# Kernel tuning notes

Hardware: AMD Instinct MI355X
Metric: run time of the kernel (lower is better)

## Reference

```python
import jax, jax.numpy as jnp
import numpy as np

N, E, L, HID, HEADS, G = 50000, 800000, 2, 128, 8, 256
DK = HID // HEADS

def _ln(x, g, b, eps=1e-5):
    m = jnp.mean(x, axis=-1, keepdims=True)
    v = jnp.mean((x - m) ** 2, axis=-1, keepdims=True)
    return (x - m) * jax.lax.rsqrt(v + eps) * g + b

def setup_inputs() -> dict:
    key = jax.random.key(0)
    ks = jax.random.split(key, 24)
    rn = lambda i, s: (0.05 * jax.random.normal(ks[i], s)).astype(jnp.float32)
    return {
        'node_attr': jax.random.randint(ks[0], (N, 4), 0, 64, dtype=jnp.int32),
        'batch_idx': jnp.sort(jax.random.randint(ks[1], (N,), 0, G, dtype=jnp.int32)),
        'edge_index': jax.random.randint(ks[2], (2, E), 0, N, dtype=jnp.int32),
        'strat_dist': jax.random.randint(ks[3], (E,), 0, 32, dtype=jnp.int32),
        'strat_path': jax.random.randint(ks[4], (E,), 0, 16, dtype=jnp.int32),
        'atom_emb': rn(5, (4, 64, HID)),
        'dist_emb': rn(6, (L, 32, HID)),
        'path_emb': rn(7, (L, 16, HID)),
        'Wq': rn(8, (L, HID, HID)), 'bq': rn(9, (L, HID)),
        'Wk': rn(10, (L, HID, HID)), 'bk': rn(11, (L, HID)),
        'Wv': rn(12, (L, HID, HID)), 'bv': rn(13, (L, HID)),
        'Wa': rn(14, (L, HID, HID)), 'ba': rn(15, (L, HID)),
        'ln1_g': jnp.ones((L, HID), jnp.float32), 'ln1_b': jnp.zeros((L, HID), jnp.float32),
        'Wmid': rn(16, (L, HID, 2 * HID)), 'bmid': rn(17, (L, 2 * HID)),
        'Wo': rn(18, (L, 2 * HID, HID)), 'bo': rn(19, (L, HID)),
        'ln2_g': jnp.ones((L, HID), jnp.float32), 'ln2_b': jnp.zeros((L, HID), jnp.float32),
        'W_out': rn(20, (HID, 1)), 'b_out': jnp.zeros((1,), jnp.float32),
    }

def reference(node_attr, batch_idx, edge_index, strat_dist, strat_path,
              atom_emb, dist_emb, path_emb, Wq, bq, Wk, bk, Wv, bv, Wa, ba,
              ln1_g, ln1_b, Wmid, bmid, Wo, bo, ln2_g, ln2_b, W_out, b_out):
    # node encoder: sum of per-feature embeddings (AtomEncoder style)
    x = sum(atom_emb[f][node_attr[:, f]] for f in range(node_attr.shape[1]))  # [N, HID]
    src, tgt = edge_index[0], edge_index[1]  # j (source), i (target)
    inv_sqrt_dk = np.float32(1.0 / np.sqrt(DK))
    for l in range(L):
        # per-edge gather + relational encodings added to the source vector
        s = x[src] + dist_emb[l][strat_dist] + path_emb[l][strat_path]  # [E, HID]
        t = x[tgt]                                                      # [E, HID]
        q = (t @ Wq[l] + bq[l]).reshape(E, HEADS, DK)
        k = (s @ Wk[l] + bk[l]).reshape(E, HEADS, DK)
        v = (s @ Wv[l] + bv[l]).reshape(E, HEADS, DK)
        scores = jnp.sum(q * k, axis=-1) * inv_sqrt_dk  # [E, HEADS]
        # segment softmax keyed on target node id
        smax = jax.ops.segment_max(scores, tgt, num_segments=N)
        ex = jnp.exp(scores - smax[tgt])
        den = jax.ops.segment_sum(ex, tgt, num_segments=N)
        att = ex / (den[tgt] + 1e-16)                   # [E, HEADS]
        msg = (v * att[:, :, None]).reshape(E, HID)
        aggr = jax.ops.segment_sum(msg, tgt, num_segments=N)  # scatter-add
        # update: attn FFN + residual + LayerNorms (dropout is identity in eval)
        h = _ln(jax.nn.gelu(aggr, approximate=False) @ Wa[l] + ba[l] + x, ln1_g[l], ln1_b[l])
        h2 = jax.nn.gelu(h @ Wmid[l] + bmid[l], approximate=False) @ Wo[l] + bo[l]
        x = _ln(h2 + h, ln2_g[l], ln2_b[l])
    # global mean pool per graph, then readout
    cnt = jax.ops.segment_sum(jnp.ones((N,), x.dtype), batch_idx, num_segments=G)
    pooled = jax.ops.segment_sum(x, batch_idx, num_segments=G) / jnp.maximum(cnt, 1.0)[:, None]
    return pooled @ W_out + b_out
```

## Files before the change

### kernel.cpp

```cpp
#include <hip/hip_runtime.h>
#include <hip/hip_bf16.h>
#include <math.h>
#include <stdint.h>

#define N_NODES 50000
#define N_EDGES 800000
#define HID 128
#define NGRAPH 256
#define NLAYER 2
#define CAP 64

#define CPAD 5

#define SC_GRP 196
#define SC_B (SC_GRP * 8)
#define NPART 6250

#define ENC_B 3125
#define TKV_B (ENC_B + 1024)
#define RPK_B (TKV_B + 128)
#define PREP_B (RPK_B + 4)

typedef __bf16 bf16x8 __attribute__((ext_vector_type(8)));
typedef __bf16 bf16x2 __attribute__((ext_vector_type(2)));
typedef float f32x4 __attribute__((ext_vector_type(4)));
typedef float f32x2 __attribute__((ext_vector_type(2)));

__device__ __forceinline__ float gelu_f(float v) {
    return 0.5f * v * (1.0f + erff(v * 0.70710678118654752f));
}

__device__ __forceinline__ f32x2 f8lo(uint32_t d) {
    return __builtin_amdgcn_cvt_pk_f32_fp8((int)d, false);
}
__device__ __forceinline__ f32x2 f8hi(uint32_t d) {
    return __builtin_amdgcn_cvt_pk_f32_fp8((int)d, true);
}
__device__ __forceinline__ uint32_t pk4_fp8(float a, float b, float c, float d) {
    int w = __builtin_amdgcn_cvt_pk_fp8_f32(a, b, 0, false);
    w = __builtin_amdgcn_cvt_pk_fp8_f32(c, d, w, true);
    return (uint32_t)w;
}
__device__ __forceinline__ f32x2 bfpair(uint32_t d) {
    f32x2 r;
    r[0] = __uint_as_float(d << 16);
    r[1] = __uint_as_float(d);
    return r;
}

__global__ __launch_bounds__(256) void prep_kernel(
    const int* __restrict__ attr, const float* __restrict__ aemb,
    __bf16* __restrict__ xb,
    const float* __restrict__ de, const float* __restrict__ pe,
    const float* __restrict__ Wk, const float* __restrict__ Wv,
    __bf16* __restrict__ tkv,
    const float* __restrict__ Wq, const float* __restrict__ Wa,
    const float* __restrict__ Wmid, const float* __restrict__ Wo,
    __bf16* __restrict__ wqkvf, __bf16* __restrict__ waf,
    __bf16* __restrict__ wmidf, __bf16* __restrict__ wof,
    const int* __restrict__ batch, const float* __restrict__ bout,
    const float* __restrict__ bq, const float* __restrict__ bk,
    const float* __restrict__ bv,
    float* __restrict__ invc, float* __restrict__ outp, float* __restrict__ bqkv,
    const int* __restrict__ tgt, const int* __restrict__ src,
    const int* __restrict__ sd, const int* __restrict__ sp,
    int* __restrict__ cnt, uint32_t* __restrict__ ei) {
    __shared__ float sde[128];
    int b = blockIdx.x;
    int tid = threadIdx.x;
    if (b < SC_B) {
        int grp = b >> 3;
        int part = b & 7;
        int plo = part * NPART;
        int phi = plo + NPART;
        int base = grp * 4096 + tid;
#pragma unroll
        for (int k = 0; k < 16; k++) {
            int e = base + k * 256;
            if (e < N_EDGES) {
                int t = tgt[e];
                if (t >= plo && t < phi) {
                    uint32_t pk = (uint32_t)src[e] | ((uint32_t)((sd[e] << 4) | sp[e]) << 16);
                    int r = atomicAdd(&cnt[t << CPAD], 1);
                    if (r < CAP) ei[(t << 6) + r] = pk;
                }
            }
        }
        return;
    }
    b -= SC_B;
    if (b < ENC_B) {
        int gid = b * 256 + tid;
        int n = gid >> 4;
        int c8 = (gid & 15) << 3;
        const int4 a = *(const int4*)(attr + n * 4);
        const float* r0 = aemb + (size_t)(0 * 64 + a.x) * 128 + c8;
        const float* r1 = aemb + (size_t)(1 * 64 + a.y) * 128 + c8;
        const float* r2 = aemb + (size_t)(2 * 64 + a.z) * 128 + c8;
        const float* r3 = aemb + (size_t)(3 * 64 + a.w) * 128 + c8;
        f32x4 v0a = *(const f32x4*)r0, v0b = *(const f32x4*)(r0 + 4);
        f32x4 v1a = *(const f32x4*)r1, v1b = *(const f32x4*)(r1 + 4);
        f32x4 v2a = *(const f32x4*)r2, v2b = *(const f32x4*)(r2 + 4);
        f32x4 v3a = *(const f32x4*)r3, v3b = *(const f32x4*)(r3 + 4);
        bf16x8 o;
#pragma unroll
        for (int j = 0; j < 4; j++) {
            o[j] = (__bf16)(v0a[j] + v1a[j] + v2a[j] + v3a[j]);
            o[4 + j] = (__bf16)(v0b[j] + v1b[j] + v2b[j] + v3b[j]);
        }
        *(bf16x8*)(xb + (size_t)n * 128 + c8) = o;
    } else if (b < TKV_B) {
        int bb = b - ENC_B;
        int l = bb >> 9;
        int md = bb & 511;
        int dd = md >> 4, pp = md & 15;
        int c = tid;
        if (c < 128) sde[c] = de[l * 4096 + dd * 128 + c] + pe[l * 2048 + pp * 128 + c];
        __syncthreads();
        const float* W = (c < 128) ? (Wk + l * 16384) : (Wv + l * 16384);
        int cc = c & 127;
        float acc = 0.f;
#pragma unroll 4
        for (int k = 0; k < 128; k++) acc = fmaf(sde[k], W[k * 128 + cc], acc);
        tkv[(size_t)bb * 256 + c] = (__bf16)acc;
    } else if (b < RPK_B) {
        int u = (b - TKV_B) * 256 + tid;
        int l = u >> 14, r = u & 16383;
        const float* srcp;
        __bf16* dstp;
        int kg, scol, srcCO;
        if (r < 6144) {
            kg = r / 384;
            int uu = r % 384;
            int sec = uu >> 7, cc = uu & 127;
            scol = ((cc & 15) << 3) | (cc >> 4);
            const float* Ws = (sec == 0) ? Wq : (sec == 1) ? Wk : Wv;
            srcp = Ws + l * 16384;
            srcCO = 128;
            dstp = wqkvf + (size_t)l * 49152 + (size_t)r * 8;
        } else if (r < 8192) {
            int rr = r - 6144;
            kg = rr >> 7;
            int cc = rr & 127;
            scol = ((cc & 15) << 3) | (cc >> 4);
            srcp = Wa + l * 16384;
            srcCO = 128;
            dstp = waf + (size_t)l * 16384 + (size_t)rr * 8;
        } else if (r < 12288) {
            int rr = r - 8192;
            kg = rr >> 8;
            int uu = rr & 255;
            int blk = uu >> 7, cc = uu & 127;
            scol = blk * 128 + (((cc & 15) << 3) | (cc >> 4));
            srcp = Wmid + l * 32768;
            srcCO = 256;
            dstp = wmidf + (size_t)l * 32768 + (size_t)rr * 8;
        } else {
            int rr = r - 12288;
            kg = rr >> 7;
            int cc = rr & 127;
            scol = ((cc & 15) << 3) | (cc >> 4);
            srcp = Wo + l * 32768;
            srcCO = 128;
            dstp = wof + (size_t)l * 32768 + (size_t)rr * 8;
        }
        bf16x8 o;
#pragma unroll
        for (int j = 0; j < 8; j++) o[j] = (__bf16)srcp[(kg * 8 + j) * srcCO + scol];
        *(bf16x8*)dstp = o;
    } else {
        int sb = b - RPK_B;
        if (sb == 0) {
            int g = tid;
            int lo = 0, hi = N_NODES;
            while (lo < hi) { int mid = (lo + hi) >> 1; if (batch[mid] < g) lo = mid + 1; else hi = mid; }
            int start = lo;
            lo = start; hi = N_NODES;
            while (lo < hi) { int mid = (lo + hi) >> 1; if (batch[mid] < g + 1) lo = mid + 1; else hi = mid; }
            int c2 = lo - start;
            invc[g] = 1.0f / fmaxf((float)c2, 1.0f);
            outp[g] = bout[0];
        } else {
            int r = (sb - 1) * 256 + tid;
            int l = r / 384, c = r % 384;
            float v = (c < 128) ? bq[l * 128 + c]
                    : (c < 256) ? bk[l * 128 + c - 128]
                                : bv[l * 128 + c - 256];
            bqkv[r] = v;
        }
    }
}

__global__ __launch_bounds__(256) void qkv_gemm(
    const __bf16* __restrict__ A, const __bf16* __restrict__ Wf,
    const float* __restrict__ bias, __bf16* __restrict__ Qb,
    uint8_t* __restrict__ kv8, int M) {
    int tid = threadIdx.x;
    int bq = blockIdx.x;
    int sec = bq % 3;
    int rowblk = bq / 3;
    int lane = tid & 63;
    int wv = tid >> 6;
    int row0 = rowblk * 64 + wv * 16;
    int col0 = sec * 128;
    if (row0 >= M) return;
    int quad = lane >> 4, tq = lane & 15;
    f32x4 acc[8] = {};
#pragma unroll
    for (int k0 = 0; k0 < 128; k0 += 32) {
        int rr = row0 + tq;
        if (rr >= M) rr = M - 1;
        bf16x8 af = *(const bf16x8*)(A + (size_t)rr * 128 + k0 + quad * 8);
#pragma unroll
        for (int nt = 0; nt < 8; nt++) {
            bf16x8 bfr = *(const bf16x8*)(Wf + ((size_t)((k0 >> 3) + quad) * 384 + col0 + nt * 16 + tq) * 8);
            acc[nt] = __builtin_amdgcn_mfma_f32_16x16x32_bf16(af, bfr, acc[nt], 0, 0, 0);
        }
    }
    int cb = tq * 8;
    float bia[8];
#pragma unroll
    for (int t = 0; t < 8; t++) bia[t] = bias[col0 + cb + t];
#pragma unroll
    for (int v = 0; v < 4; v++) {
        int rr = row0 + quad * 4 + v;
        if (rr >= M) continue;
        float val[8];
#pragma unroll
        for (int t = 0; t < 8; t++) val[t] = acc[t][v] + bia[t];
        if (sec == 0) {
            bf16x8 ov;
#pragma unroll
            for (int t = 0; t < 8; t++) ov[t] = (__bf16)val[t];
            *(bf16x8*)(Qb + (size_t)rr * 128 + cb) = ov;
        } else {
            uint2 st;
            st.x = pk4_fp8(val[0], val[1], val[2], val[3]);
            st.y = pk4_fp8(val[4], val[5], val[6], val[7]);
            *(uint2*)(kv8 + (size_t)rr * 256 + (sec - 1) * 128 + cb) = st;
        }
    }
}

template <bool POOL>
__global__ __launch_bounds__(256) void ffn_uber(
    const __bf16* __restrict__ A,
    const __bf16* __restrict__ xres,
    const __bf16* __restrict__ Waf, const float* __restrict__ ba,
    const float* __restrict__ l1g, const float* __restrict__ l1b,
    const __bf16* __restrict__ Wmf, const float* __restrict__ bmid,
    const __bf16* __restrict__ Wof, const float* __restrict__ bo,
    const float* __restrict__ l2g, const float* __restrict__ l2b,
    __bf16* __restrict__ outx,
    const int* __restrict__ batch, const float* __restrict__ invc,
    const float* __restrict__ WoutV, float* __restrict__ outp,
    int M) {
    __shared__ __bf16 hld[4][16][136];
    __shared__ __bf16 smid[4][16][264];
    __shared__ float ps[POOL ? NGRAPH : 1];
    int lane = threadIdx.x & 63;
    int wv = threadIdx.x >> 6;
    int row0 = blockIdx.x * 64 + wv * 16;
    bool active = row0 < M;
    if (POOL) {
        ps[threadIdx.x] = 0.f;
        __syncthreads();
    } else if (!active) {
        return;
    }
    int quad = lane >> 4, tq = lane & 15;
    if (active) {
        int cb = tq * 8;
        {
            f32x4 acc[8] = {};
#pragma unroll
            for (int k0 = 0; k0 < 128; k0 += 32) {
                int rr = row0 + tq;
                if (rr >= M) rr = M - 1;
                bf16x8 af = *(const bf16x8*)(A + (size_t)rr * 128 + k0 + quad * 8);
#pragma unroll
                for (int nt = 0; nt < 8; nt++) {
                    bf16x8 bfr = *(const bf16x8*)(Waf + ((size_t)((k0 >> 3) + quad) * 128 + nt * 16 + tq) * 8);
                    acc[nt] = __builtin_amdgcn_mfma_f32_16x16x32_bf16(af, bfr, acc[nt], 0, 0, 0);
                }
            }
            float bia[8], gv[8], bv2[8];
#pragma unroll
            for (int t = 0; t < 8; t++) {
                bia[t] = ba[cb + t];
                gv[t] = l1g[cb + t];
                bv2[t] = l1b[cb + t];
            }
#pragma unroll
            for (int v = 0; v < 4; v++) {
                int rr = row0 + quad * 4 + v;
                int rc = (rr < M) ? rr : M - 1;
                bf16x8 rv = *(const bf16x8*)(xres + (size_t)rc * 128 + cb);
                float val[8];
#pragma unroll
                for (int t = 0; t < 8; t++) val[t] = acc[t][v] + bia[t] + (float)rv[t];
                float s = 0.f, s2 = 0.f;
#pragma unroll
                for (int t = 0; t < 8; t++) { s += val[t]; s2 = fmaf(val[t], val[t], s2); }
#pragma unroll
                for (int o = 1; o < 16; o <<= 1) {
                    s += __shfl_xor(s, o);
                    s2 += __shfl_xor(s2, o);
                }
                float m = s * (1.0f / 128.0f);
                float var = s2 * (1.0f / 128.0f) - m * m;
                float rs = rsqrtf(var + 1e-5f);
                bf16x8 ov;
#pragma unroll
                for (int t = 0; t < 8; t++) ov[t] = (__bf16)((val[t] - m) * rs * gv[t] + bv2[t]);
                *(bf16x8*)(&hld[wv][quad * 4 + v][cb]) = ov;
            }
        }
        asm volatile("" ::: "memory");
#pragma unroll
        for (int cH = 0; cH < 2; ++cH) {
            f32x4 acc[8] = {};
#pragma unroll
            for (int k0 = 0; k0 < 128; k0 += 32) {
                bf16x8 af = *(const bf16x8*)(&hld[wv][tq][k0 + quad * 8]);
#pragma unroll
                for (int nt = 0; nt < 8; nt++) {
                    bf16x8 bfr = *(const bf16x8*)(Wmf + ((size_t)((k0 >> 3) + quad) * 256 + cH * 128 + nt * 16 + tq) * 8);
                    acc[nt] = __builtin_amdgcn_mfma_f32_16x16x32_bf16(af, bfr, acc[nt], 0, 0, 0);
                }
            }
            int cb2 = cH * 128 + cb;
            float bia[8];
#pragma unroll
            for (int t = 0; t < 8; t++) bia[t] = bmid[cb2 + t];
#pragma unroll
            for (int v = 0; v < 4; v++) {
                bf16x8 ov;
#pragma unroll
                for (int t = 0; t < 8; t++) ov[t] = (__bf16)gelu_f(acc[t][v] + bia[t]);
                *(bf16x8*)(&smid[wv][quad * 4 + v][cb2]) = ov;
            }
        }
        asm volatile("" ::: "memory");
        f32x4 acc[8] = {};
#pragma unroll
        for (int k0 = 0; k0 < 256; k0 += 32) {
            bf16x8 af = *(const bf16x8*)(&smid[wv][tq][k0 + quad * 8]);
#pragma unroll
            for (int nt = 0; nt < 8; nt++) {
                bf16x8 bfr = *(const bf16x8*)(Wof + ((size_t)((k0 >> 3) + quad) * 128 + nt * 16 + tq) * 8);
                acc[nt] = __builtin_amdgcn_mfma_f32_16x16x32_bf16(af, bfr, acc[nt], 0, 0, 0);
            }
        }
        float bia[8], gv[8], bv2[8], wo8[8];
#pragma unroll
        for (int t = 0; t < 8; t++) {
            bia[t] = bo[cb + t];
            gv[t] = l2g[cb + t];
            bv2[t] = l2b[cb + t];
        }
        if (POOL) {
#pragma unroll
            for (int t = 0; t < 8; t++) wo8[t] = WoutV[cb + t];
        }
#pragma unroll
        for (int v = 0; v < 4; v++) {
            int rr = row0 + quad * 4 + v;
            bf16x8 rv = *(const bf16x8*)(&hld[wv][quad * 4 + v][cb]);
            float val[8];
#pragma unroll
            for (int t = 0; t < 8; t++) val[t] = acc[t][v] + bia[t] + (float)rv[t];
            float s = 0.f, s2 = 0.f;
#pragma unroll
            for (int t = 0; t < 8; t++) { s += val[t]; s2 = fmaf(val[t], val[t], s2); }
#pragma unroll
            for (int o = 1; o < 16; o <<= 1) {
                s += __shfl_xor(s, o);
                s2 += __shfl_xor(s2, o);
            }
            float m = s * (1.0f / 128.0f);
            float var = s2 * (1.0f / 128.0f) - m * m;
            float rs = rsqrtf(var + 1e-5f);
#pragma unroll
            for (int t = 0; t < 8; t++) val[t] = (val[t] - m) * rs * gv[t] + bv2[t];
            if (rr >= M) continue;
            if (!POOL) {
                bf16x8 ov;
#pragma unroll
                for (int t = 0; t < 8; t++) ov[t] = (__bf16)val[t];
                *(bf16x8*)(outx + (size_t)rr * 128 + cb) = ov;
            } else {
                float dot = 0.f;
#pragma unroll
                for (int t = 0; t < 8; t++) dot = fmaf(val[t], wo8[t], dot);
#pragma unroll
                for (int o = 1; o < 16; o <<= 1) dot += __shfl_xor(dot, o);
                if (tq == 0) {
                    int g = batch[rr];
                    atomicAdd(&ps[g], dot * invc[g]);
                }
            }
        }
    }
    if (POOL) {
        __syncthreads();
        float pv = ps[threadIdx.x];
        if (pv != 0.f) atomicAdd(&outp[threadIdx.x], pv);
    }
}

__global__ __launch_bounds__(256) void attn_kernel(
    const __bf16* __restrict__ Qb, const uint8_t* __restrict__ kv8,
    const __bf16* __restrict__ tkv,
    const int* __restrict__ cnt, const uint32_t* __restrict__ ei,
    __bf16* __restrict__ outb) {
    __shared__ float red[4][1376];
    int wv = threadIdx.x >> 6;
    int i = blockIdx.x * 4 + wv;
    int lane = threadIdx.x & 63;
    int slot = lane >> 3, h = lane & 7;
    int ch0 = h * 16;
    const uint4* qv = (const uint4*)(Qb + (size_t)i * 128 + ch0);
    uint4 qa = qv[0], qb = qv[1];
    uint32_t qd[8] = {qa.x, qa.y, qa.z, qa.w, qb.x, qb.y, qb.z, qb.w};
    f32x2 qp[8];
#pragma unroll
    for (int j = 0; j < 8; j++) qp[j] = bfpair(qd[j]);
    int deg = cnt[i << CPAD];
    if (deg > CAP) deg = CAP;
    int p0 = i << 6;
    int p1 = p0 + deg;
    float l = 0.f;
    f32x2 ap[8] = {};
    int p = p0 + slot;
    uint32_t w1 = 0, w2 = 0;
    if (p < p1) w1 = ei[p];
    if (p + 8 < p1) w2 = ei[p + 8];
    uint4 kw, vw, t0, t1, u0, u1;
    {
        int j = w1 & 0xffff, md = w1 >> 16;
        const uint8_t* kr = kv8 + (size_t)j * 256 + ch0;
        kw = *(const uint4*)kr;
        vw = *(const uint4*)(kr + 128);
        const __bf16* tr = tkv + md * 256 + ch0;
        t0 = *(const uint4*)tr;
        t1 = *(const uint4*)(tr + 8);
        u0 = *(const uint4*)(tr + 128);
        u1 = *(const uint4*)(tr + 136);
    }
    while (p < p1) {
        uint4 kwn, vwn, t0n, t1n, u0n, u1n;
        {
            int j = w2 & 0xffff, md = w2 >> 16;
            const uint8_t* kr = kv8 + (size_t)j * 256 + ch0;
            kwn = *(const uint4*)kr;
            vwn = *(const uint4*)(kr + 128);
            const __bf16* tr = tkv + md * 256 + ch0;
            t0n = *(const uint4*)tr;
            t1n = *(const uint4*)(tr + 8);
            u0n = *(const uint4*)(tr + 128);
            u1n = *(const uint4*)(tr + 136);
        }
        int pn = p + 16;
        uint32_t w3 = ei[(pn < p1) ? pn : p];
        uint32_t kd[4] = {kw.x, kw.y, kw.z, kw.w};
        uint32_t vd[4] = {vw.x, vw.y, vw.z, vw.w};
        uint32_t td[8] = {t0.x, t0.y, t0.z, t0.w, t1.x, t1.y, t1.z, t1.w};
        uint32_t ud[8] = {u0.x, u0.y, u0.z, u0.w, u1.x, u1.y, u1.z, u1.w};
        f32x2 sa = {0.f, 0.f};
#pragma unroll
        for (int j = 0; j < 4; j++) {
            f32x2 klo = f8lo(kd[j]) + bfpair(td[2 * j]);
            f32x2 khi = f8hi(kd[j]) + bfpair(td[2 * j + 1]);
            sa = qp[2 * j] * klo + sa;
            sa = qp[2 * j + 1] * khi + sa;
        }
        float s = sa[0] + sa[1];
        float pe = __expf(s * 0.25f);
        l += pe;
        f32x2 pp = {pe, pe};
#pragma unroll
        for (int j = 0; j < 4; j++) {
            f32x2 vlo = f8lo(vd[j]) + bfpair(ud[2 * j]);
            f32x2 vhi = f8hi(vd[j]) + bfpair(ud[2 * j + 1]);
            ap[2 * j] = pp * vlo + ap[2 * j];
            ap[2 * j + 1] = pp * vhi + ap[2 * j + 1];
        }
        kw = kwn; vw = vwn; t0 = t0n; t1 = t1n; u0 = u0n; u1 = u1n;
        w2 = w3;
        p += 8;
    }
    float* rw = red[wv] + slot * 172 + 20 * h;
#pragma unroll
    for (int j = 0; j < 8; j++) *(f32x2*)(rw + 2 * j) = ap[j];
    red[wv][slot * 172 + 156 + h] = l;
    asm volatile("" ::: "memory");
    int pc = 2 * lane + 4 * (lane >> 3);
    int hh = lane >> 3;
    float s0 = 0.f, s1 = 0.f, ls = 0.f;
#pragma unroll
    for (int s = 0; s < 8; s++) {
        float2 v = *(const float2*)(red[wv] + s * 172 + pc);
        s0 += v.x;
        s1 += v.y;
        ls += red[wv][s * 172 + 156 + hh];
    }
    float inv = 1.0f / (ls + 1e-16f);
    bf16x2 o2;
    o2[0] = (__bf16)gelu_f(s0 * inv);
    o2[1] = (__bf16)gelu_f(s1 * inv);
    *(bf16x2*)(outb + (size_t)i * 128 + 2 * lane) = o2;
}

extern "C" void kernel_launch(void* const* d_in, const int* in_sizes, int n_in,
                              void* d_out, int out_size, void* d_ws, size_t ws_size,
                              hipStream_t stream) {
    const int N = N_NODES, E = N_EDGES;
    const int* node_attr = (const int*)d_in[0];
    const int* batch_idx = (const int*)d_in[1];
    const int* edge_index = (const int*)d_in[2];
    const int* strat_dist = (const int*)d_in[3];
    const int* strat_path = (const int*)d_in[4];
    const float* atom_emb = (const float*)d_in[5];
    const float* dist_emb = (const float*)d_in[6];
    const float* path_emb = (const float*)d_in[7];
    const float* Wq = (const float*)d_in[8];
    const float* bq = (const float*)d_in[9];
    const float* Wk = (const float*)d_in[10];
    const float* bk = (const float*)d_in[11];
    const float* Wv = (const float*)d_in[12];
    const float* bv = (const float*)d_in[13];
    const float* Wa = (const float*)d_in[14];
    const float* ba = (const float*)d_in[15];
    const float* ln1g = (const float*)d_in[16];
    const float* ln1b = (const float*)d_in[17];
    const float* Wmid = (const float*)d_in[18];
    const float* bmid = (const float*)d_in[19];
    const float* Wo = (const float*)d_in[20];
    const float* bo = (const float*)d_in[21];
    const float* ln2g = (const float*)d_in[22];
    const float* ln2b = (const float*)d_in[23];
    const float* Wout = (const float*)d_in[24];
    const float* bout = (const float*)d_in[25];
    float* out = (float*)d_out;

    const int* src = edge_index;
    const int* tgt = edge_index + E;

    size_t NF = (size_t)N * HID;
    float* invc = (float*)d_ws;
    float* bqkv = invc + 256;
    __bf16* xb = (__bf16*)(bqkv + 768);
    __bf16* Qb = xb + NF;
    __bf16* ab = Qb + NF;
    __bf16* tkv = ab + NF;
    __bf16* wqkvf = tkv + 262144;
    __bf16* waf = wqkvf + 98304;
    __bf16* wmidf = waf + 32768;
    __bf16* wof = wmidf + 65536;
    uint8_t* kv8 = (uint8_t*)(wof + 65536);
    uint32_t* ei = (uint32_t*)(kv8 + (size_t)N * 256);
    int* cnt = (int*)(ei + (size_t)N * CAP);

    hipMemsetAsync(cnt, 0, (size_t)N * 32 * sizeof(int), stream);
    prep_kernel<<<SC_B + PREP_B, 256, 0, stream>>>(
        node_attr, atom_emb, xb,
        dist_emb, path_emb, Wk, Wv, tkv,
        Wq, Wa, Wmid, Wo, wqkvf, waf, wmidf, wof,
        batch_idx, bout, bq, bk, bv, invc, out, bqkv,
        tgt, src, strat_dist, strat_path, cnt, ei);

    const int GB = (N + 63) / 64;
    const int AB = (N + 3) / 4;

    for (int l = 0; l < NLAYER; ++l) {
        qkv_gemm<<<3 * GB, 256, 0, stream>>>(
            xb, wqkvf + l * 49152, bqkv + l * 384, Qb, kv8, N);

        attn_kernel<<<AB, 256, 0, stream>>>(Qb, kv8, tkv + l * 131072, cnt, ei, ab);

        if (l < NLAYER - 1) {
            ffn_uber<false><<<GB, 256, 0, stream>>>(
                ab, xb, waf + l * 16384, ba + l * 128, ln1g + l * 128, ln1b + l * 128,
                wmidf + l * 32768, bmid + l * 256, wof + l * 32768, bo + l * 128,
                ln2g + l * 128, ln2b + l * 128, xb,
                nullptr, nullptr, nullptr, nullptr, N);
        } else {
            ffn_uber<true><<<GB, 256, 0, stream>>>(
                ab, xb, waf + l * 16384, ba + l * 128, ln1g + l * 128, ln1b + l * 128,
                wmidf + l * 32768, bmid + l * 256, wof + l * 32768, bo + l * 128,
                ln2g + l * 128, ln2b + l * 128, nullptr,
                batch_idx, invc, Wout, out, N);
        }
    }
}
```

Baseline: 370.1 us.

## Bin edges by target in LDS per block instead of global atomics

Edge binning by target node now uses 196 blocks. Each block owns 256 target nodes, scans all edge targets, and fills a shared-memory adjacency table using LDS atomics, then writes it out with coalesced stores. This replaces global atomics on padded counters, and with it the memset and the 8-way partition scan. Edge fields are pre-packed into one word by a separate earlier kernel, so setup now takes two launches. Each binning block reads the full target array (about 3.2MB) and holds 64KB of LDS, which limits occupancy and multiplies global reads.

Result: slower. 706.0 us (+90.8%).

```diff
diff --git a/kernel.cpp b/kernel.cpp
--- a/kernel.cpp
+++ b/kernel.cpp
@@ -10,16 +10,15 @@
 #define NLAYER 2
 #define CAP 64
 
-#define CPAD 5
-
-#define SC_GRP 196
-#define SC_B (SC_GRP * 8)
-#define NPART 6250
+#define BIN_B 196
+#define N_PAD (BIN_B * 256)
 
 #define ENC_B 3125
 #define TKV_B (ENC_B + 1024)
-#define RPK_B (TKV_B + 128)
-#define PREP_B (RPK_B + 4)
+#define PREP1_B (TKV_B)
+
+#define PK_B 782
+#define PREP0_B (132 + PK_B)
 
 typedef __bf16 bf16x8 __attribute__((ext_vector_type(8)));
 typedef __bf16 bf16x2 __attribute__((ext_vector_type(2)));
@@ -48,83 +47,22 @@
     return r;
 }
 
-__global__ __launch_bounds__(256) void prep_kernel(
-    const int* __restrict__ attr, const float* __restrict__ aemb,
-    __bf16* __restrict__ xb,
-    const float* __restrict__ de, const float* __restrict__ pe,
-    const float* __restrict__ Wk, const float* __restrict__ Wv,
-    __bf16* __restrict__ tkv,
+__global__ __launch_bounds__(256) void prep0_kernel(
     const float* __restrict__ Wq, const float* __restrict__ Wa,
     const float* __restrict__ Wmid, const float* __restrict__ Wo,
+    const float* __restrict__ Wk, const float* __restrict__ Wv,
     __bf16* __restrict__ wqkvf, __bf16* __restrict__ waf,
     __bf16* __restrict__ wmidf, __bf16* __restrict__ wof,
     const int* __restrict__ batch, const float* __restrict__ bout,
     const float* __restrict__ bq, const float* __restrict__ bk,
     const float* __restrict__ bv,
     float* __restrict__ invc, float* __restrict__ outp, float* __restrict__ bqkv,
-    const int* __restrict__ tgt, const int* __restrict__ src,
-    const int* __restrict__ sd, const int* __restrict__ sp,
-    int* __restrict__ cnt, uint32_t* __restrict__ ei) {
-    __shared__ float sde[128];
+    const int* __restrict__ src, const int* __restrict__ sd,
+    const int* __restrict__ sp, uint32_t* __restrict__ pack) {
     int b = blockIdx.x;
     int tid = threadIdx.x;
-    if (b < SC_B) {
-        int grp = b >> 3;
-        int part = b & 7;
-        int plo = part * NPART;
-        int phi = plo + NPART;
-        int base = grp * 4096 + tid;
-#pragma unroll
-        for (int k = 0; k < 16; k++) {
-            int e = base + k * 256;
-            if (e < N_EDGES) {
-                int t = tgt[e];
-                if (t >= plo && t < phi) {
-                    uint32_t pk = (uint32_t)src[e] | ((uint32_t)((sd[e] << 4) | sp[e]) << 16);
-                    int r = atomicAdd(&cnt[t << CPAD], 1);
-                    if (r < CAP) ei[(t << 6) + r] = pk;
-                }
-            }
-        }
-        return;
-    }
-    b -= SC_B;
-    if (b < ENC_B) {
-        int gid = b * 256 + tid;
-        int n = gid >> 4;
-        int c8 = (gid & 15) << 3;
-        const int4 a = *(const int4*)(attr + n * 4);
-        const float* r0 = aemb + (size_t)(0 * 64 + a.x) * 128 + c8;
-        const float* r1 = aemb + (size_t)(1 * 64 + a.y) * 128 + c8;
-        const float* r2 = aemb + (size_t)(2 * 64 + a.z) * 128 + c8;
-        const float* r3 = aemb + (size_t)(3 * 64 + a.w) * 128 + c8;
-        f32x4 v0a = *(const f32x4*)r0, v0b = *(const f32x4*)(r0 + 4);
-        f32x4 v1a = *(const f32x4*)r1, v1b = *(const f32x4*)(r1 + 4);
-        f32x4 v2a = *(const f32x4*)r2, v2b = *(const f32x4*)(r2 + 4);
-        f32x4 v3a = *(const f32x4*)r3, v3b = *(const f32x4*)(r3 + 4);
-        bf16x8 o;
-#pragma unroll
-        for (int j = 0; j < 4; j++) {
-            o[j] = (__bf16)(v0a[j] + v1a[j] + v2a[j] + v3a[j]);
-            o[4 + j] = (__bf16)(v0b[j] + v1b[j] + v2b[j] + v3b[j]);
-        }
-        *(bf16x8*)(xb + (size_t)n * 128 + c8) = o;
-    } else if (b < TKV_B) {
-        int bb = b - ENC_B;
-        int l = bb >> 9;
-        int md = bb & 511;
-        int dd = md >> 4, pp = md & 15;
-        int c = tid;
-        if (c < 128) sde[c] = de[l * 4096 + dd * 128 + c] + pe[l * 2048 + pp * 128 + c];
-        __syncthreads();
-        const float* W = (c < 128) ? (Wk + l * 16384) : (Wv + l * 16384);
-        int cc = c & 127;
-        float acc = 0.f;
-#pragma unroll 4
-        for (int k = 0; k < 128; k++) acc = fmaf(sde[k], W[k * 128 + cc], acc);
-        tkv[(size_t)bb * 256 + c] = (__bf16)acc;
-    } else if (b < RPK_B) {
-        int u = (b - TKV_B) * 256 + tid;
+    if (b < 128) {
+        int u = b * 256 + tid;
         int l = u >> 14, r = u & 16383;
         const float* srcp;
         __bf16* dstp;
@@ -168,8 +106,8 @@
 #pragma unroll
         for (int j = 0; j < 8; j++) o[j] = (__bf16)srcp[(kg * 8 + j) * srcCO + scol];
         *(bf16x8*)dstp = o;
-    } else {
-        int sb = b - RPK_B;
+    } else if (b < 132) {
+        int sb = b - 128;
         if (sb == 0) {
             int g = tid;
             int lo = 0, hi = N_NODES;
@@ -188,6 +126,115 @@
                                 : bv[l * 128 + c - 256];
             bqkv[r] = v;
         }
+    } else {
+        int e0 = (b - 132) * 1024 + tid * 4;
+        if (e0 + 3 < N_EDGES) {
+            int4 s4 = *(const int4*)(src + e0);
+            int4 d4 = *(const int4*)(sd + e0);
+            int4 p4 = *(const int4*)(sp + e0);
+            uint4 o;
+            o.x = (uint32_t)s4.x | ((uint32_t)((d4.x << 4) | p4.x) << 16);
+            o.y = (uint32_t)s4.y | ((uint32_t)((d4.y << 4) | p4.y) << 16);
+            o.z = (uint32_t)s4.z | ((uint32_t)((d4.z << 4) | p4.z) << 16);
+            o.w = (uint32_t)s4.w | ((uint32_t)((d4.w << 4) | p4.w) << 16);
+            *(uint4*)(pack + e0) = o;
+        } else {
+            for (int j = 0; j < 4; j++) {
+                int e = e0 + j;
+                if (e < N_EDGES)
+                    pack[e] = (uint32_t)src[e] | ((uint32_t)((sd[e] << 4) | sp[e]) << 16);
+            }
+        }
+    }
+}
+
+__global__ __launch_bounds__(256) void prep1_kernel(
+    const int* __restrict__ attr, const float* __restrict__ aemb,
+    __bf16* __restrict__ xb,
+    const float* __restrict__ de, const float* __restrict__ pe,
+    const float* __restrict__ Wk, const float* __restrict__ Wv,
+    __bf16* __restrict__ tkv,
+    const int* __restrict__ tgt, const uint32_t* __restrict__ pack,
+    int* __restrict__ cnt, uint32_t* __restrict__ ei) {
+    int b = blockIdx.x;
+    int tid = threadIdx.x;
+    if (b < BIN_B) {
+        __shared__ int lcnt[256];
+        __shared__ uint32_t lei[256 * CAP];
+        int lo = b << 8;
+        lcnt[tid] = 0;
+        __syncthreads();
+        for (int it = 0; it < 782; ++it) {
+            int e0 = it * 1024 + tid * 4;
+            if (e0 + 3 < N_EDGES) {
+                int4 tg = *(const int4*)(tgt + e0);
+#pragma unroll
+                for (int j = 0; j < 4; j++) {
+                    int t = (j == 0) ? tg.x : (j == 1) ? tg.y : (j == 2) ? tg.z : tg.w;
+                    unsigned tl = (unsigned)(t - lo);
+                    if (tl < 256u) {
+                        int r = atomicAdd(&lcnt[tl], 1);
+                        if (r < CAP) lei[(tl << 6) + r] = pack[e0 + j];
+                    }
+                }
+            } else if (e0 < N_EDGES) {
+                for (int j = 0; j < 4 && e0 + j < N_EDGES; j++) {
+                    int t = tgt[e0 + j];
+                    unsigned tl = (unsigned)(t - lo);
+                    if (tl < 256u) {
+                        int r = atomicAdd(&lcnt[tl], 1);
+                        if (r < CAP) lei[(tl << 6) + r] = pack[e0 + j];
+                    }
+                }
+            }
+        }
+        __syncthreads();
+        int t = lo + tid;
+        if (t < N_NODES) cnt[t] = min(lcnt[tid], CAP);
+        uint32_t* gout = ei + ((size_t)lo << 6);
+#pragma unroll
+        for (int i = 0; i < 16; ++i) {
+            int w = i * 1024 + tid * 4;
+            *(uint4*)(gout + w) = *(const uint4*)(lei + w);
+        }
+        return;
+    }
+    b -= BIN_B;
+    if (b < ENC_B) {
+        int gid = b * 256 + tid;
+        int n = gid >> 4;
+        int c8 = (gid & 15) << 3;
+        const int4 a = *(const int4*)(attr + n * 4);
+        const float* r0 = aemb + (size_t)(0 * 64 + a.x) * 128 + c8;
+        const float* r1 = aemb + (size_t)(1 * 64 + a.y) * 128 + c8;
+        const float* r2 = aemb + (size_t)(2 * 64 + a.z) * 128 + c8;
+        const float* r3 = aemb + (size_t)(3 * 64 + a.w) * 128 + c8;
+        f32x4 v0a = *(const f32x4*)r0, v0b = *(const f32x4*)(r0 + 4);
+        f32x4 v1a = *(const f32x4*)r1, v1b = *(const f32x4*)(r1 + 4);
+        f32x4 v2a = *(const f32x4*)r2, v2b = *(const f32x4*)(r2 + 4);
+        f32x4 v3a = *(const f32x4*)r3, v3b = *(const f32x4*)(r3 + 4);
+        bf16x8 o;
+#pragma unroll
+        for (int j = 0; j < 4; j++) {
+            o[j] = (__bf16)(v0a[j] + v1a[j] + v2a[j] + v3a[j]);
+            o[4 + j] = (__bf16)(v0b[j] + v1b[j] + v2b[j] + v3b[j]);
+        }
+        *(bf16x8*)(xb + (size_t)n * 128 + c8) = o;
+    } else {
+        __shared__ float sde[128];
+        int bb = b - ENC_B;
+        int l = bb >> 9;
+        int md = bb & 511;
+        int dd = md >> 4, pp = md & 15;
+        int c = tid;
+        if (c < 128) sde[c] = de[l * 4096 + dd * 128 + c] + pe[l * 2048 + pp * 128 + c];
+        __syncthreads();
+        const float* W = (c < 128) ? (Wk + l * 16384) : (Wv + l * 16384);
+        int cc = c & 127;
+        float acc = 0.f;
+#pragma unroll 4
+        for (int k = 0; k < 128; k++) acc = fmaf(sde[k], W[k * 128 + cc], acc);
+        tkv[(size_t)bb * 256 + c] = (__bf16)acc;
     }
 }
 
@@ -426,7 +473,7 @@
     f32x2 qp[8];
 #pragma unroll
     for (int j = 0; j < 8; j++) qp[j] = bfpair(qd[j]);
-    int deg = cnt[i << CPAD];
+    int deg = cnt[i];
     if (deg > CAP) deg = CAP;
     int p0 = i << 6;
     int p1 = p0 + deg;
@@ -560,15 +607,16 @@
     __bf16* wof = wmidf + 65536;
     uint8_t* kv8 = (uint8_t*)(wof + 65536);
     uint32_t* ei = (uint32_t*)(kv8 + (size_t)N * 256);
-    int* cnt = (int*)(ei + (size_t)N * CAP);
-
-    hipMemsetAsync(cnt, 0, (size_t)N * 32 * sizeof(int), stream);
-    prep_kernel<<<SC_B + PREP_B, 256, 0, stream>>>(
-        node_attr, atom_emb, xb,
-        dist_emb, path_emb, Wk, Wv, tkv,
-        Wq, Wa, Wmid, Wo, wqkvf, waf, wmidf, wof,
+    uint32_t* pack = ei + (size_t)N_PAD * CAP;
+    int* cnt = (int*)(pack + N_EDGES);
+
+    prep0_kernel<<<PREP0_B, 256, 0, stream>>>(
+        Wq, Wa, Wmid, Wo, Wk, Wv, wqkvf, waf, wmidf, wof,
         batch_idx, bout, bq, bk, bv, invc, out, bqkv,
-        tgt, src, strat_dist, strat_path, cnt, ei);
+        src, strat_dist, strat_path, pack);
+    prep1_kernel<<<BIN_B + PREP1_B, 256, 0, stream>>>(
+        node_attr, atom_emb, xb, dist_emb, path_emb, Wk, Wv, tkv,
+        tgt, pack, cnt, ei);
 
     const int GB = (N + 63) / 64;
     const int AB = (N + 3) / 4;
```

## Pack degree counters densely and reduce attention partials with wave shuffles

Applied to the files above, without the earlier changes.

Drops the 32-int padding on the per-node degree counters, so the memset and the counter reads and atomics touch 32x less memory, at the cost of more atomic contention per cache line. Replaces the LDS-based cross-slot reduction in the attention kernel with a butterfly of xor shuffles across the 8 edge slots, then each lane selects its own channel pair. This removes the 22KB of shared memory per block (raising occupancy) but adds many cross-lane shuffle instructions.

Result: no change. 364.6 us (-1.5%).

```diff
diff --git a/kernel.cpp b/kernel.cpp
--- a/kernel.cpp
+++ b/kernel.cpp
@@ -9,8 +9,6 @@
 #define NGRAPH 256
 #define NLAYER 2
 #define CAP 64
-
-#define CPAD 5
 
 #define SC_GRP 196
 #define SC_B (SC_GRP * 8)
@@ -81,7 +79,7 @@
                 int t = tgt[e];
                 if (t >= plo && t < phi) {
                     uint32_t pk = (uint32_t)src[e] | ((uint32_t)((sd[e] << 4) | sp[e]) << 16);
-                    int r = atomicAdd(&cnt[t << CPAD], 1);
+                    int r = atomicAdd(&cnt[t], 1);
                     if (r < CAP) ei[(t << 6) + r] = pk;
                 }
             }
@@ -414,7 +412,6 @@
     const __bf16* __restrict__ tkv,
     const int* __restrict__ cnt, const uint32_t* __restrict__ ei,
     __bf16* __restrict__ outb) {
-    __shared__ float red[4][1376];
     int wv = threadIdx.x >> 6;
     int i = blockIdx.x * 4 + wv;
     int lane = threadIdx.x & 63;
@@ -426,7 +423,7 @@
     f32x2 qp[8];
 #pragma unroll
     for (int j = 0; j < 8; j++) qp[j] = bfpair(qd[j]);
-    int deg = cnt[i << CPAD];
+    int deg = cnt[i];
     if (deg > CAP) deg = CAP;
     int p0 = i << 6;
     int p1 = p0 + deg;
@@ -490,26 +487,27 @@
         w2 = w3;
         p += 8;
     }
-    float* rw = red[wv] + slot * 172 + 20 * h;
-#pragma unroll
-    for (int j = 0; j < 8; j++) *(f32x2*)(rw + 2 * j) = ap[j];
-    red[wv][slot * 172 + 156 + h] = l;
-    asm volatile("" ::: "memory");
-    int pc = 2 * lane + 4 * (lane >> 3);
-    int hh = lane >> 3;
-    float s0 = 0.f, s1 = 0.f, ls = 0.f;
-#pragma unroll
-    for (int s = 0; s < 8; s++) {
-        float2 v = *(const float2*)(red[wv] + s * 172 + pc);
-        s0 += v.x;
-        s1 += v.y;
-        ls += red[wv][s * 172 + 156 + hh];
-    }
-    float inv = 1.0f / (ls + 1e-16f);
+#pragma unroll
+    for (int m = 8; m <= 32; m <<= 1) {
+        l += __shfl_xor(l, m);
+#pragma unroll
+        for (int j = 0; j < 8; j++) {
+            f32x2 o;
+            o[0] = __shfl_xor(ap[j][0], m);
+            o[1] = __shfl_xor(ap[j][1], m);
+            ap[j] = ap[j] + o;
+        }
+    }
+    float inv = 1.0f / (l + 1e-16f);
+    float v0 = ap[0][0], v1 = ap[0][1];
+#pragma unroll
+    for (int j = 1; j < 8; j++) {
+        if (slot == j) { v0 = ap[j][0]; v1 = ap[j][1]; }
+    }
     bf16x2 o2;
-    o2[0] = (__bf16)gelu_f(s0 * inv);
-    o2[1] = (__bf16)gelu_f(s1 * inv);
-    *(bf16x2*)(outb + (size_t)i * 128 + 2 * lane) = o2;
+    o2[0] = (__bf16)gelu_f(v0 * inv);
+    o2[1] = (__bf16)gelu_f(v1 * inv);
+    *(bf16x2*)(outb + (size_t)i * 128 + ch0 + slot * 2) = o2;
 }
 
 extern "C" void kernel_launch(void* const* d_in, const int* in_sizes, int n_in,
@@ -562,7 +560,7 @@
     uint32_t* ei = (uint32_t*)(kv8 + (size_t)N * 256);
     int* cnt = (int*)(ei + (size_t)N * CAP);
 
-    hipMemsetAsync(cnt, 0, (size_t)N * 32 * sizeof(int), stream);
+    hipMemsetAsync(cnt, 0, (size_t)N * sizeof(int), stream);
     prep_kernel<<<SC_B + PREP_B, 256, 0, stream>>>(
         node_attr, atom_emb, xb,
         dist_emb, path_emb, Wk, Wv, tkv,
```
